# Kernel optimization log

Measured on AMD Instinct MI355X. Metric: run time of the kernel, lower is better.

The kernel has to match this reference:

```python
import jax, jax.numpy as jnp
import numpy as np

NEG_INF = -1e30  # stands in for float('-inf'); avoids nan in masked softmax edge cases


def setup_inputs() -> dict:
    key = jax.random.key(0)
    ks = jax.random.split(key, 6)
    B, N, MD, QD, AD = 64, 512, 1024, 1024, 1024
    stdv_m = 1.0 / np.sqrt(MD)
    stdv_q = 1.0 / np.sqrt(QD)
    stdv_a = 1.0 / np.sqrt(AD)
    return {
        "memory_values": jax.random.normal(ks[0], (B, N, MD), dtype=jnp.float32),
        "mask": jax.random.randint(ks[1], (B, N), 0, 2, dtype=jnp.int32),
        "query": jax.random.normal(ks[2], (B, QD), dtype=jnp.float32),
        "Wh": jax.random.uniform(ks[3], (MD, AD), jnp.float32, -stdv_m, stdv_m),
        "Ws": jax.random.uniform(ks[4], (QD, AD), jnp.float32, -stdv_q, stdv_q),
        "v": jax.random.uniform(ks[5], (AD, 1), jnp.float32, -stdv_a, stdv_a),
    }


def reference(memory_values, mask, query, Wh, Ws, v):
    # Et(i) = tanh(Hi*Wh + St*Ws) @ v ; At = softmax(Et) with masking
    tq = query @ Ws                                   # (B, AD)
    h = jnp.tanh(memory_values @ Wh + tq[:, None, :])  # (B, N, AD)
    logits = jnp.squeeze(h @ v, axis=-1)              # (B, N)

    maskf = mask.astype(logits.dtype)
    # no_cells[b] == 1 iff every cell in row b is masked out
    no_cells = jnp.prod(1.0 - maskf, axis=1, keepdims=True)  # (B, 1)
    suppress = jnp.where(maskf == 0, NEG_INF, 0.0)
    suppress = jnp.where(no_cells == 1.0, 0.0, suppress)
    weights = jax.nn.softmax(logits + suppress, axis=-1)
    weights = jnp.where(no_cells == 1.0, 0.0, weights)

    context = jnp.einsum("bn,bnd->bd", weights, memory_values)
    return context
```

## Files before the change

### kernel.cpp

```cpp
#include <hip/hip_runtime.h>
#include <cstdint>
#include <cstddef>

typedef float floatx4 __attribute__((ext_vector_type(4)));
typedef _Float16 half8_t __attribute__((ext_vector_type(8)));
typedef _Float16 half2_t __attribute__((ext_vector_type(2)));

#define AS1 __attribute__((address_space(1)))
#define AS3 __attribute__((address_space(3)))

__device__ __forceinline__ void glds16(const void* g, void* l) {
  __builtin_amdgcn_global_load_lds((const AS1 void*)g, (AS3 void*)l, 16, 0, 0);
}

__device__ __forceinline__ half2_t pkrtz(float a, float b) {
  return __builtin_bit_cast(half2_t, __builtin_amdgcn_cvt_pkrtz(a, b));
}

__device__ __forceinline__ float fast_tanh(float x) {
  float e2 = __expf(2.f * x);
  return 1.f - 2.f * __builtin_amdgcn_rcpf(e2 + 1.f);
}

__global__ void kp_cvt(const float* __restrict__ mem, _Float16* __restrict__ memh) {
  size_t i = ((size_t)(blockIdx.x << 8) + threadIdx.x) << 3;
  floatx4 a = *(const floatx4*)(mem + i);
  floatx4 b = *(const floatx4*)(mem + i + 4);
  union { half2_t h2[4]; half8_t h8; } u;
  u.h2[0] = half2_t{(_Float16)a[0], (_Float16)a[1]};
  u.h2[1] = half2_t{(_Float16)a[2], (_Float16)a[3]};
  u.h2[2] = half2_t{(_Float16)b[0], (_Float16)b[1]};
  u.h2[3] = half2_t{(_Float16)b[2], (_Float16)b[3]};
  *(half8_t*)(memh + i) = u.h8;
}

__global__ void k0_transpose(const float* __restrict__ Wh, _Float16* __restrict__ WhT) {
  __shared__ float t[64][65];
  int k0 = blockIdx.y << 6, n0 = blockIdx.x << 6;
  int tx = threadIdx.x, ty = threadIdx.y;
  #pragma unroll
  for (int r = ty; r < 64; r += 4) t[r][tx] = Wh[(size_t)(k0 + r) * 1024 + n0 + tx];
  __syncthreads();
  #pragma unroll
  for (int r = ty; r < 64; r += 4)
    WhT[(size_t)(n0 + r) * 1024 + k0 + tx] = (_Float16)t[tx][r];
}

__global__ __launch_bounds__(256) void k1a_tq(const float* __restrict__ q,
                                              const float* __restrict__ Ws,
                                              float* __restrict__ tqp) {
  __shared__ float qts[64][68];
  __shared__ float wss[64][68];
  const int db = blockIdx.x << 6, kb = blockIdx.y << 6;
  const int tid = threadIdx.x;
  for (int idx = tid; idx < 4096; idx += 256) {
    int b = idx >> 6, kk = idx & 63;
    qts[kk][b] = q[(b << 10) + kb + kk];
  }
  for (int idx = tid; idx < 4096; idx += 256) {
    int kk = idx >> 6, dd = idx & 63;
    wss[kk][dd] = Ws[(size_t)(kb + kk) * 1024 + db + dd];
  }
  __syncthreads();
  const int bq = tid >> 4, dq = tid & 15;
  floatx4 acc[4] = {{0.f, 0.f, 0.f, 0.f}, {0.f, 0.f, 0.f, 0.f},
                    {0.f, 0.f, 0.f, 0.f}, {0.f, 0.f, 0.f, 0.f}};
  for (int kk = 0; kk < 64; ++kk) {
    floatx4 wv = *(const floatx4*)&wss[kk][dq << 2];
    floatx4 qv = *(const floatx4*)&qts[kk][bq << 2];
    #pragma unroll
    for (int bb = 0; bb < 4; ++bb) acc[bb] += qv[bb] * wv;
  }
  #pragma unroll
  for (int bb = 0; bb < 4; ++bb) {
    int b = (bq << 2) + bb;
    *(floatx4*)(tqp + ((size_t)blockIdx.y << 16) + (b << 10) + db + (dq << 2)) = acc[bb];
  }
}

__global__ void k1b_red(const float* __restrict__ tqp, float* __restrict__ tq) {
  int i = (blockIdx.x << 8) + threadIdx.x;
  float s = 0.f;
  #pragma unroll
  for (int kc = 0; kc < 16; ++kc) s += tqp[((size_t)kc << 16) + i];
  tq[i] = s;
}

__global__ __launch_bounds__(256) void k1_tq(const float* __restrict__ q,
                                             const float* __restrict__ Ws,
                                             float* __restrict__ tq) {
  __shared__ float qs[1024];
  __shared__ float red[4][64];
  int b = blockIdx.y;
  int d0 = blockIdx.x << 6;
  int dl = threadIdx.x & 63, kg = threadIdx.x >> 6;
  for (int k = threadIdx.x; k < 1024; k += 256) qs[k] = q[(b << 10) + k];
  __syncthreads();
  float acc = 0.f;
  int kbase = kg << 8;
  #pragma unroll 8
  for (int k = 0; k < 256; ++k)
    acc += qs[kbase + k] * Ws[(size_t)(kbase + k) * 1024 + d0 + dl];
  red[kg][dl] = acc;
  __syncthreads();
  if (kg == 0)
    tq[(b << 10) + d0 + dl] = red[0][dl] + red[1][dl] + red[2][dl] + red[3][dl];
}

__global__ __launch_bounds__(256, 2) void k2_gemm_h(
    const _Float16* __restrict__ Ah, const _Float16* __restrict__ BT,
    const float* __restrict__ tq, const float* __restrict__ v,
    float* __restrict__ partials) {
  __shared__ _Float16 As[128 * 32];
  __shared__ _Float16 Bs[128 * 32];
  const int bid = blockIdx.x;
  const int mtile = ((bid >> 6) << 3) | (bid & 7);
  const int nblk = (bid >> 3) & 7;
  const int m0 = mtile << 7, n0 = nblk << 7;
  const int tid = threadIdx.x;
  const int w = tid >> 6, lane = tid & 63;
  const int wm = w >> 1, wn = w & 1, quad = lane >> 4, l15 = lane & 15;

  floatx4 acc[4][4];
  #pragma unroll
  for (int i = 0; i < 4; ++i)
    #pragma unroll
    for (int j = 0; j < 4; ++j) acc[i][j] = floatx4{0.f, 0.f, 0.f, 0.f};

  const _Float16 *gA[2], *gB[2];
  _Float16 *lA[2], *lB[2];
  #pragma unroll
  for (int t = 0; t < 2; ++t) {
    int L = (t << 8) + (w << 6) + lane;
    int row = L >> 2, jj = L & 3;
    int j = (jj - row - (row >> 2)) & 3;
    gA[t] = Ah + (size_t)(m0 + row) * 1024 + (j << 3);
    gB[t] = BT + (size_t)(n0 + row) * 1024 + (j << 3);
    lA[t] = As + (t << 11) + (w << 9);
    lB[t] = Bs + (t << 11) + (w << 9);
  }

  const half8_t *aaddr[4], *baddr[4];
  #pragma unroll
  for (int i = 0; i < 4; ++i) {
    int ar = (wm << 6) + (i << 4) + l15;
    aaddr[i] = (const half8_t*)(As + (ar << 5) + (((quad + ar + (ar >> 2)) & 3) << 3));
    int br = (wn << 6) + (i << 4) + l15;
    baddr[i] = (const half8_t*)(Bs + (br << 5) + (((quad + br + (br >> 2)) & 3) << 3));
  }

  for (int k0 = 0; k0 < 1024; k0 += 32) {
    __syncthreads();
    glds16(gA[0] + k0, lA[0]);
    glds16(gA[1] + k0, lA[1]);
    glds16(gB[0] + k0, lB[0]);
    glds16(gB[1] + k0, lB[1]);
    __syncthreads();
    half8_t af[4], bfr[4];
    #pragma unroll
    for (int i = 0; i < 4; ++i) af[i] = *aaddr[i];
    #pragma unroll
    for (int j = 0; j < 4; ++j) bfr[j] = *baddr[j];
    #pragma unroll
    for (int i = 0; i < 4; ++i)
      #pragma unroll
      for (int j = 0; j < 4; ++j)
        acc[i][j] = __builtin_amdgcn_mfma_f32_16x16x32_f16(af[i], bfr[j], acc[i][j], 0, 0, 0);
  }

  const int b = m0 >> 9;
  const int colbase = n0 + (wn << 6) + l15;
  float tqv[4], vv[4];
  #pragma unroll
  for (int j = 0; j < 4; ++j) {
    int n = colbase + (j << 4);
    tqv[j] = tq[(b << 10) + n];
    vv[j] = v[n];
  }
  #pragma unroll
  for (int i = 0; i < 4; ++i) {
    #pragma unroll
    for (int r = 0; r < 4; ++r) {
      float s = 0.f;
      #pragma unroll
      for (int j = 0; j < 4; ++j) s += fast_tanh(acc[i][j][r] + tqv[j]) * vv[j];
      s += __shfl_xor(s, 1);
      s += __shfl_xor(s, 2);
      s += __shfl_xor(s, 4);
      s += __shfl_xor(s, 8);
      if (l15 == 0) {
        int m = m0 + (wm << 6) + (i << 4) + (quad << 2) + r;
        partials[m * 16 + (nblk << 1) + wn] = s;
      }
    }
  }
}

__global__ __launch_bounds__(256, 2) void k2_gemm_f32(
    const float* __restrict__ A, const _Float16* __restrict__ BT,
    const float* __restrict__ tq, const float* __restrict__ v,
    float* __restrict__ partials) {
  __shared__ float As[128 * 32];
  __shared__ _Float16 Bs[128 * 32];
  const int bid = blockIdx.x;
  const int mtile = ((bid >> 6) << 3) | (bid & 7);
  const int nblk = (bid >> 3) & 7;
  const int m0 = mtile << 7, n0 = nblk << 7;
  const int tid = threadIdx.x;
  const int w = tid >> 6, lane = tid & 63;
  const int wm = w >> 1, wn = w & 1, quad = lane >> 4, l15 = lane & 15;

  floatx4 acc[4][4];
  #pragma unroll
  for (int i = 0; i < 4; ++i)
    #pragma unroll
    for (int j = 0; j < 4; ++j) acc[i][j] = floatx4{0.f, 0.f, 0.f, 0.f};

  const float* gA[4];
  float* lA[4];
  #pragma unroll
  for (int t = 0; t < 4; ++t) {
    int L = (t << 8) + (w << 6) + lane;
    int row = L >> 3, jj = L & 7;
    int j = (jj - row) & 7;
    gA[t] = A + (size_t)(m0 + row) * 1024 + (j << 2);
    lA[t] = As + (t << 10) + (w << 8);
  }
  const _Float16* gB[2];
  _Float16* lB[2];
  #pragma unroll
  for (int t = 0; t < 2; ++t) {
    int L = (t << 8) + (w << 6) + lane;
    int row = L >> 2, jj = L & 3;
    int j = (jj - row - (row >> 2)) & 3;
    gB[t] = BT + (size_t)(n0 + row) * 1024 + (j << 3);
    lB[t] = Bs + (t << 11) + (w << 9);
  }
  const floatx4* aaddr[4][2];
  #pragma unroll
  for (int i = 0; i < 4; ++i) {
    int row = (wm << 6) + (i << 4) + l15;
    #pragma unroll
    for (int h = 0; h < 2; ++h) {
      int pos = ((quad << 1) + h + row) & 7;
      aaddr[i][h] = (const floatx4*)(As + (row << 5) + (pos << 2));
    }
  }
  const half8_t* baddr[4];
  #pragma unroll
  for (int j = 0; j < 4; ++j) {
    int row = (wn << 6) + (j << 4) + l15;
    int pos = (quad + row + (row >> 2)) & 3;
    baddr[j] = (const half8_t*)(Bs + (row << 5) + (pos << 3));
  }
  for (int k0 = 0; k0 < 1024; k0 += 32) {
    __syncthreads();
    glds16(gA[0] + k0, lA[0]);
    glds16(gA[1] + k0, lA[1]);
    glds16(gA[2] + k0, lA[2]);
    glds16(gA[3] + k0, lA[3]);
    glds16(gB[0] + k0, lB[0]);
    glds16(gB[1] + k0, lB[1]);
    __syncthreads();
    half8_t af[4], bfr[4];
    #pragma unroll
    for (int i = 0; i < 4; ++i) {
      floatx4 x = *aaddr[i][0], y = *aaddr[i][1];
      union { half2_t h2[4]; half8_t h8; } u;
      u.h2[0] = pkrtz(x[0], x[1]);
      u.h2[1] = pkrtz(x[2], x[3]);
      u.h2[2] = pkrtz(y[0], y[1]);
      u.h2[3] = pkrtz(y[2], y[3]);
      af[i] = u.h8;
    }
    #pragma unroll
    for (int j = 0; j < 4; ++j) bfr[j] = *baddr[j];
    #pragma unroll
    for (int i = 0; i < 4; ++i)
      #pragma unroll
      for (int j = 0; j < 4; ++j)
        acc[i][j] = __builtin_amdgcn_mfma_f32_16x16x32_f16(af[i], bfr[j], acc[i][j], 0, 0, 0);
  }
  const int b = m0 >> 9;
  const int colbase = n0 + (wn << 6) + l15;
  float tqv[4], vv[4];
  #pragma unroll
  for (int j = 0; j < 4; ++j) {
    int n = colbase + (j << 4);
    tqv[j] = tq[(b << 10) + n];
    vv[j] = v[n];
  }
  #pragma unroll
  for (int i = 0; i < 4; ++i) {
    #pragma unroll
    for (int r = 0; r < 4; ++r) {
      float s = 0.f;
      #pragma unroll
      for (int j = 0; j < 4; ++j) s += fast_tanh(acc[i][j][r] + tqv[j]) * vv[j];
      s += __shfl_xor(s, 1);
      s += __shfl_xor(s, 2);
      s += __shfl_xor(s, 4);
      s += __shfl_xor(s, 8);
      if (l15 == 0) {
        int m = m0 + (wm << 6) + (i << 4) + (quad << 2) + r;
        partials[m * 16 + (nblk << 1) + wn] = s;
      }
    }
  }
}

__global__ __launch_bounds__(512) void k3_softmax(const float* __restrict__ partials,
                                                  const int* __restrict__ mask,
                                                  float* __restrict__ weights) {
  int b = blockIdx.x;
  int n = threadIdx.x;
  int m = (b << 9) + n;
  float s = 0.f;
  #pragma unroll
  for (int i = 0; i < 16; ++i) s += partials[m * 16 + i];
  int mk = mask[m];
  float logit = mk ? s : -1e30f;
  __shared__ float red[8];
  float x = logit;
  #pragma unroll
  for (int off = 32; off > 0; off >>= 1) x = fmaxf(x, __shfl_xor(x, off));
  if ((n & 63) == 0) red[n >> 6] = x;
  __syncthreads();
  float mx = red[0];
  #pragma unroll
  for (int i = 1; i < 8; ++i) mx = fmaxf(mx, red[i]);
  float e = mk ? __expf(logit - mx) : 0.f;
  float ss = e;
  #pragma unroll
  for (int off = 32; off > 0; off >>= 1) ss += __shfl_xor(ss, off);
  __syncthreads();
  if ((n & 63) == 0) red[n >> 6] = ss;
  __syncthreads();
  float tot = 0.f;
  #pragma unroll
  for (int i = 0; i < 8; ++i) tot += red[i];
  weights[m] = (tot > 0.f) ? e / tot : 0.f;
}

__global__ void k4_ctx_h(const _Float16* __restrict__ memh,
                         const float* __restrict__ weights, float* __restrict__ ctxp) {
  int nc = blockIdx.x, b = blockIdx.y;
  int d = threadIdx.x << 3;
  float acc[8] = {0.f, 0.f, 0.f, 0.f, 0.f, 0.f, 0.f, 0.f};
  int nbase = nc << 5;
  for (int n = nbase; n < nbase + 32; ++n) {
    float wv = weights[(b << 9) + n];
    half8_t x = *(const half8_t*)(memh + ((size_t)((b << 9) + n) << 10) + d);
    #pragma unroll
    for (int k = 0; k < 8; ++k) acc[k] += wv * (float)x[k];
  }
  float* o = ctxp + ((size_t)((b << 4) + nc) << 10) + d;
  #pragma unroll
  for (int k = 0; k < 8; ++k) o[k] = acc[k];
}

__global__ void k5_reduce16(const float* __restrict__ ctxp, float* __restrict__ out) {
  int i = (blockIdx.x << 8) + threadIdx.x;
  int b = i >> 10, d = i & 1023;
  float s = 0.f;
  #pragma unroll
  for (int cc = 0; cc < 16; ++cc) s += ctxp[((size_t)((b << 4) + cc) << 10) + d];
  out[i] = s;
}

__global__ void k4_ctx_f32(const float* __restrict__ mem, const float* __restrict__ weights,
                           float* __restrict__ ctxp) {
  int nc = blockIdx.x, b = blockIdx.y;
  int d = threadIdx.x << 3;
  floatx4 a0 = {0.f, 0.f, 0.f, 0.f}, a1 = {0.f, 0.f, 0.f, 0.f};
  int nbase = nc << 6;
  for (int n = nbase; n < nbase + 64; ++n) {
    float wv = weights[(b << 9) + n];
    const floatx4* p = (const floatx4*)(mem + ((size_t)((b << 9) + n) << 10) + d);
    a0 += wv * p[0];
    a1 += wv * p[1];
  }
  floatx4* o = (floatx4*)(ctxp + ((size_t)((b << 3) + nc) << 10) + d);
  o[0] = a0;
  o[1] = a1;
}

__global__ void k5_reduce8(const float* __restrict__ ctxp, float* __restrict__ out) {
  int i = (blockIdx.x << 8) + threadIdx.x;
  int b = i >> 10, d = i & 1023;
  float s = 0.f;
  #pragma unroll
  for (int cc = 0; cc < 8; ++cc) s += ctxp[((size_t)((b << 3) + cc) << 10) + d];
  out[i] = s;
}

extern "C" void kernel_launch(void* const* d_in, const int* in_sizes, int n_in,
                              void* d_out, int out_size, void* d_ws, size_t ws_size,
                              hipStream_t stream) {
  const float* mem = (const float*)d_in[0];
  const int* mask = (const int*)d_in[1];
  const float* query = (const float*)d_in[2];
  const float* Wh = (const float*)d_in[3];
  const float* Ws = (const float*)d_in[4];
  const float* v = (const float*)d_in[5];
  float* out = (float*)d_out;

  char* ws = (char*)d_ws;
  const size_t need16 = (73ull << 20);

  if (ws_size >= need16) {
    _Float16* memh = (_Float16*)ws;
    _Float16* WhT = (_Float16*)(ws + (64ull << 20));
    float* partials = (float*)(ws + (66ull << 20));
    float* tq = (float*)(ws + (68ull << 20));
    float* weights = (float*)(ws + (68ull << 20) + (256 << 10));
    float* ctxp = (float*)(ws + (69ull << 20));
    float* tqp = ctxp;

    kp_cvt<<<16384, 256, 0, stream>>>(mem, memh);
    k0_transpose<<<dim3(16, 16), dim3(64, 4), 0, stream>>>(Wh, WhT);
    k1a_tq<<<dim3(16, 16), 256, 0, stream>>>(query, Ws, tqp);
    k1b_red<<<256, 256, 0, stream>>>(tqp, tq);
    k2_gemm_h<<<2048, 256, 0, stream>>>(memh, WhT, tq, v, partials);
    k3_softmax<<<64, 512, 0, stream>>>(partials, mask, weights);
    k4_ctx_h<<<dim3(16, 64), 128, 0, stream>>>(memh, weights, ctxp);
    k5_reduce16<<<256, 256, 0, stream>>>(ctxp, out);
  } else {
    _Float16* WhT = (_Float16*)ws;
    float* partials = (float*)(ws + ((size_t)2 << 20));
    float* tq = (float*)(ws + ((size_t)4 << 20));
    float* weights = (float*)(ws + ((size_t)4 << 20) + (256 << 10));
    float* ctxp = (float*)(ws + ((size_t)9 << 19));

    k0_transpose<<<dim3(16, 16), dim3(64, 4), 0, stream>>>(Wh, WhT);
    k1_tq<<<dim3(16, 64), 256, 0, stream>>>(query, Ws, tq);
    k2_gemm_f32<<<2048, 256, 0, stream>>>(mem, WhT, tq, v, partials);
    k3_softmax<<<64, 512, 0, stream>>>(partials, mask, weights);
    k4_ctx_f32<<<dim3(8, 64), 128, 0, stream>>>(mem, weights, ctxp);
    k5_reduce8<<<256, 256, 0, stream>>>(ctxp, out);
  }
}
```

Measured before the change: 338.5 us.

## Fuse prep kernels into one launch and fold tq reduction into GEMM

Merges the fp16 conversion of memory, the Wh transpose and the partial query projection into a single heterogeneous kernel that dispatches on block index, removing three launches and the separate tq reduction kernel. The GEMM kernel now sums the 16 tq partials itself in its prologue, which adds some redundant global reads per block. The context kernel is reshaped to 256 threads with 64 rows per chunk and 8 partials, which halves the final reduction input. The transpose blocks are now serialized over 16 k-tiles each, so only 16 blocks do that work and they may form a long tail.

```diff
diff --git a/kernel.cpp b/kernel.cpp
--- a/kernel.cpp
+++ b/kernel.cpp
@@ -4,6 +4,7 @@
 
 typedef float floatx4 __attribute__((ext_vector_type(4)));
 typedef _Float16 half8_t __attribute__((ext_vector_type(8)));
+typedef _Float16 half4_t __attribute__((ext_vector_type(4)));
 typedef _Float16 half2_t __attribute__((ext_vector_type(2)));
 
 #define AS1 __attribute__((address_space(1)))
@@ -22,94 +23,77 @@
   return 1.f - 2.f * __builtin_amdgcn_rcpf(e2 + 1.f);
 }
 
-__global__ void kp_cvt(const float* __restrict__ mem, _Float16* __restrict__ memh) {
-  size_t i = ((size_t)(blockIdx.x << 8) + threadIdx.x) << 3;
-  floatx4 a = *(const floatx4*)(mem + i);
-  floatx4 b = *(const floatx4*)(mem + i + 4);
-  union { half2_t h2[4]; half8_t h8; } u;
-  u.h2[0] = half2_t{(_Float16)a[0], (_Float16)a[1]};
-  u.h2[1] = half2_t{(_Float16)a[2], (_Float16)a[3]};
-  u.h2[2] = half2_t{(_Float16)b[0], (_Float16)b[1]};
-  u.h2[3] = half2_t{(_Float16)b[2], (_Float16)b[3]};
-  *(half8_t*)(memh + i) = u.h8;
-}
-
-__global__ void k0_transpose(const float* __restrict__ Wh, _Float16* __restrict__ WhT) {
-  __shared__ float t[64][65];
-  int k0 = blockIdx.y << 6, n0 = blockIdx.x << 6;
-  int tx = threadIdx.x, ty = threadIdx.y;
-  #pragma unroll
-  for (int r = ty; r < 64; r += 4) t[r][tx] = Wh[(size_t)(k0 + r) * 1024 + n0 + tx];
-  __syncthreads();
-  #pragma unroll
-  for (int r = ty; r < 64; r += 4)
-    WhT[(size_t)(n0 + r) * 1024 + k0 + tx] = (_Float16)t[tx][r];
-}
-
-__global__ __launch_bounds__(256) void k1a_tq(const float* __restrict__ q,
-                                              const float* __restrict__ Ws,
-                                              float* __restrict__ tqp) {
-  __shared__ float qts[64][68];
-  __shared__ float wss[64][68];
-  const int db = blockIdx.x << 6, kb = blockIdx.y << 6;
+__global__ __launch_bounds__(256) void k_prep(
+    const float* __restrict__ mem, const float* __restrict__ Wh,
+    const float* __restrict__ q, const float* __restrict__ Ws,
+    _Float16* __restrict__ memh, _Float16* __restrict__ WhT,
+    float* __restrict__ tqp) {
+  __shared__ union {
+    float t[64][65];
+    struct { float qts[64][68]; float wss[64][68]; } k1;
+  } sm;
+  const int bx = blockIdx.x;
   const int tid = threadIdx.x;
-  for (int idx = tid; idx < 4096; idx += 256) {
-    int b = idx >> 6, kk = idx & 63;
-    qts[kk][b] = q[(b << 10) + kb + kk];
-  }
-  for (int idx = tid; idx < 4096; idx += 256) {
-    int kk = idx >> 6, dd = idx & 63;
-    wss[kk][dd] = Ws[(size_t)(kb + kk) * 1024 + db + dd];
-  }
-  __syncthreads();
-  const int bq = tid >> 4, dq = tid & 15;
-  floatx4 acc[4] = {{0.f, 0.f, 0.f, 0.f}, {0.f, 0.f, 0.f, 0.f},
-                    {0.f, 0.f, 0.f, 0.f}, {0.f, 0.f, 0.f, 0.f}};
-  for (int kk = 0; kk < 64; ++kk) {
-    floatx4 wv = *(const floatx4*)&wss[kk][dq << 2];
-    floatx4 qv = *(const floatx4*)&qts[kk][bq << 2];
-    #pragma unroll
-    for (int bb = 0; bb < 4; ++bb) acc[bb] += qv[bb] * wv;
-  }
-  #pragma unroll
-  for (int bb = 0; bb < 4; ++bb) {
-    int b = (bq << 2) + bb;
-    *(floatx4*)(tqp + ((size_t)blockIdx.y << 16) + (b << 10) + db + (dq << 2)) = acc[bb];
-  }
-}
-
-__global__ void k1b_red(const float* __restrict__ tqp, float* __restrict__ tq) {
-  int i = (blockIdx.x << 8) + threadIdx.x;
-  float s = 0.f;
-  #pragma unroll
-  for (int kc = 0; kc < 16; ++kc) s += tqp[((size_t)kc << 16) + i];
-  tq[i] = s;
-}
-
-__global__ __launch_bounds__(256) void k1_tq(const float* __restrict__ q,
-                                             const float* __restrict__ Ws,
-                                             float* __restrict__ tq) {
-  __shared__ float qs[1024];
-  __shared__ float red[4][64];
-  int b = blockIdx.y;
-  int d0 = blockIdx.x << 6;
-  int dl = threadIdx.x & 63, kg = threadIdx.x >> 6;
-  for (int k = threadIdx.x; k < 1024; k += 256) qs[k] = q[(b << 10) + k];
-  __syncthreads();
-  float acc = 0.f;
-  int kbase = kg << 8;
-  #pragma unroll 8
-  for (int k = 0; k < 256; ++k)
-    acc += qs[kbase + k] * Ws[(size_t)(kbase + k) * 1024 + d0 + dl];
-  red[kg][dl] = acc;
-  __syncthreads();
-  if (kg == 0)
-    tq[(b << 10) + d0 + dl] = red[0][dl] + red[1][dl] + red[2][dl] + red[3][dl];
+
+  if (bx < 8192) {
+    size_t base = ((size_t)bx << 12);
+    #pragma unroll
+    for (int p = 0; p < 4; ++p) {
+      size_t i = base + (p << 10) + (tid << 2);
+      floatx4 x = *(const floatx4*)(mem + i);
+      half4_t h = {(_Float16)x[0], (_Float16)x[1], (_Float16)x[2], (_Float16)x[3]};
+      *(half4_t*)(memh + i) = h;
+    }
+  } else if (bx < 8208) {
+    const int n0 = (bx - 8192) << 6;
+    const int c = tid & 63, rr = tid >> 6;
+    for (int kt = 0; kt < 16; ++kt) {
+      int k0 = kt << 6;
+      #pragma unroll
+      for (int i = 0; i < 16; ++i) {
+        int r = (i << 2) + rr;
+        sm.t[r][c] = Wh[(size_t)(k0 + r) * 1024 + n0 + c];
+      }
+      __syncthreads();
+      #pragma unroll
+      for (int i = 0; i < 16; ++i) {
+        int r = (i << 2) + rr;
+        WhT[(size_t)(n0 + r) * 1024 + k0 + c] = (_Float16)sm.t[c][r];
+      }
+      __syncthreads();
+    }
+  } else {
+    const int bid2 = bx - 8208;
+    const int db = (bid2 & 15) << 6, kb = (bid2 >> 4) << 6;
+    for (int idx = tid; idx < 4096; idx += 256) {
+      int b = idx >> 6, kk = idx & 63;
+      sm.k1.qts[kk][b] = q[(b << 10) + kb + kk];
+    }
+    for (int idx = tid; idx < 4096; idx += 256) {
+      int kk = idx >> 6, dd = idx & 63;
+      sm.k1.wss[kk][dd] = Ws[(size_t)(kb + kk) * 1024 + db + dd];
+    }
+    __syncthreads();
+    const int bq = tid >> 4, dq = tid & 15;
+    floatx4 acc[4] = {{0.f, 0.f, 0.f, 0.f}, {0.f, 0.f, 0.f, 0.f},
+                      {0.f, 0.f, 0.f, 0.f}, {0.f, 0.f, 0.f, 0.f}};
+    for (int kk = 0; kk < 64; ++kk) {
+      floatx4 wv = *(const floatx4*)&sm.k1.wss[kk][dq << 2];
+      floatx4 qv = *(const floatx4*)&sm.k1.qts[kk][bq << 2];
+      #pragma unroll
+      for (int bb = 0; bb < 4; ++bb) acc[bb] += qv[bb] * wv;
+    }
+    #pragma unroll
+    for (int bb = 0; bb < 4; ++bb) {
+      int b = (bq << 2) + bb;
+      *(floatx4*)(tqp + ((size_t)(bid2 >> 4) << 16) + (b << 10) + db + (dq << 2)) = acc[bb];
+    }
+  }
 }
 
 __global__ __launch_bounds__(256, 2) void k2_gemm_h(
     const _Float16* __restrict__ Ah, const _Float16* __restrict__ BT,
-    const float* __restrict__ tq, const float* __restrict__ v,
+    const float* __restrict__ tqp, const float* __restrict__ v,
     float* __restrict__ partials) {
   __shared__ _Float16 As[128 * 32];
   __shared__ _Float16 Bs[128 * 32];
@@ -121,6 +105,19 @@
   const int w = tid >> 6, lane = tid & 63;
   const int wm = w >> 1, wn = w & 1, quad = lane >> 4, l15 = lane & 15;
 
+  const int b = m0 >> 9;
+  const int colbase = n0 + (wn << 6) + l15;
+  float tqv[4], vv[4];
+  #pragma unroll
+  for (int j = 0; j < 4; ++j) {
+    int n = colbase + (j << 4);
+    float s = 0.f;
+    #pragma unroll
+    for (int p = 0; p < 16; ++p) s += tqp[(p << 16) + (b << 10) + n];
+    tqv[j] = s;
+    vv[j] = v[n];
+  }
+
   floatx4 acc[4][4];
   #pragma unroll
   for (int i = 0; i < 4; ++i)
@@ -168,15 +165,6 @@
         acc[i][j] = __builtin_amdgcn_mfma_f32_16x16x32_f16(af[i], bfr[j], acc[i][j], 0, 0, 0);
   }
 
-  const int b = m0 >> 9;
-  const int colbase = n0 + (wn << 6) + l15;
-  float tqv[4], vv[4];
-  #pragma unroll
-  for (int j = 0; j < 4; ++j) {
-    int n = colbase + (j << 4);
-    tqv[j] = tq[(b << 10) + n];
-    vv[j] = v[n];
-  }
   #pragma unroll
   for (int i = 0; i < 4; ++i) {
     #pragma unroll
@@ -194,6 +182,99 @@
       }
     }
   }
+}
+
+__global__ __launch_bounds__(512) void k3_softmax(const float* __restrict__ partials,
+                                                  const int* __restrict__ mask,
+                                                  float* __restrict__ weights) {
+  int b = blockIdx.x;
+  int n = threadIdx.x;
+  int m = (b << 9) + n;
+  float s = 0.f;
+  #pragma unroll
+  for (int i = 0; i < 16; ++i) s += partials[m * 16 + i];
+  int mk = mask[m];
+  float logit = mk ? s : -1e30f;
+  __shared__ float red[8];
+  float x = logit;
+  #pragma unroll
+  for (int off = 32; off > 0; off >>= 1) x = fmaxf(x, __shfl_xor(x, off));
+  if ((n & 63) == 0) red[n >> 6] = x;
+  __syncthreads();
+  float mx = red[0];
+  #pragma unroll
+  for (int i = 1; i < 8; ++i) mx = fmaxf(mx, red[i]);
+  float e = mk ? __expf(logit - mx) : 0.f;
+  float ss = e;
+  #pragma unroll
+  for (int off = 32; off > 0; off >>= 1) ss += __shfl_xor(ss, off);
+  __syncthreads();
+  if ((n & 63) == 0) red[n >> 6] = ss;
+  __syncthreads();
+  float tot = 0.f;
+  #pragma unroll
+  for (int i = 0; i < 8; ++i) tot += red[i];
+  weights[m] = (tot > 0.f) ? e / tot : 0.f;
+}
+
+__global__ __launch_bounds__(256) void k4_ctx_h(const _Float16* __restrict__ memh,
+                                                const float* __restrict__ weights,
+                                                float* __restrict__ ctxp) {
+  int nc = blockIdx.x, b = blockIdx.y;
+  int d = threadIdx.x << 2;
+  float a0 = 0.f, a1 = 0.f, a2 = 0.f, a3 = 0.f;
+  int nbase = nc << 6;
+  for (int n = nbase; n < nbase + 64; ++n) {
+    float wv = weights[(b << 9) + n];
+    half4_t x = *(const half4_t*)(memh + ((size_t)((b << 9) + n) << 10) + d);
+    a0 += wv * (float)x[0];
+    a1 += wv * (float)x[1];
+    a2 += wv * (float)x[2];
+    a3 += wv * (float)x[3];
+  }
+  *(floatx4*)(ctxp + ((size_t)((b << 3) + nc) << 10) + d) = floatx4{a0, a1, a2, a3};
+}
+
+__global__ void k5_reduce8(const float* __restrict__ ctxp, float* __restrict__ out) {
+  int i = (blockIdx.x << 8) + threadIdx.x;
+  int b = i >> 10, d = i & 1023;
+  float s = 0.f;
+  #pragma unroll
+  for (int cc = 0; cc < 8; ++cc) s += ctxp[((size_t)((b << 3) + cc) << 10) + d];
+  out[i] = s;
+}
+
+__global__ void k0_transpose(const float* __restrict__ Wh, _Float16* __restrict__ WhT) {
+  __shared__ float t[64][65];
+  int k0 = blockIdx.y << 6, n0 = blockIdx.x << 6;
+  int tx = threadIdx.x, ty = threadIdx.y;
+  #pragma unroll
+  for (int r = ty; r < 64; r += 4) t[r][tx] = Wh[(size_t)(k0 + r) * 1024 + n0 + tx];
+  __syncthreads();
+  #pragma unroll
+  for (int r = ty; r < 64; r += 4)
+    WhT[(size_t)(n0 + r) * 1024 + k0 + tx] = (_Float16)t[tx][r];
+}
+
+__global__ __launch_bounds__(256) void k1_tq(const float* __restrict__ q,
+                                             const float* __restrict__ Ws,
+                                             float* __restrict__ tq) {
+  __shared__ float qs[1024];
+  __shared__ float red[4][64];
+  int b = blockIdx.y;
+  int d0 = blockIdx.x << 6;
+  int dl = threadIdx.x & 63, kg = threadIdx.x >> 6;
+  for (int k = threadIdx.x; k < 1024; k += 256) qs[k] = q[(b << 10) + k];
+  __syncthreads();
+  float acc = 0.f;
+  int kbase = kg << 8;
+  #pragma unroll 8
+  for (int k = 0; k < 256; ++k)
+    acc += qs[kbase + k] * Ws[(size_t)(kbase + k) * 1024 + d0 + dl];
+  red[kg][dl] = acc;
+  __syncthreads();
+  if (kg == 0)
+    tq[(b << 10) + d0 + dl] = red[0][dl] + red[1][dl] + red[2][dl] + red[3][dl];
 }
 
 __global__ __launch_bounds__(256, 2) void k2_gemm_f32(
@@ -209,13 +290,11 @@
   const int tid = threadIdx.x;
   const int w = tid >> 6, lane = tid & 63;
   const int wm = w >> 1, wn = w & 1, quad = lane >> 4, l15 = lane & 15;
-
   floatx4 acc[4][4];
   #pragma unroll
   for (int i = 0; i < 4; ++i)
     #pragma unroll
     for (int j = 0; j < 4; ++j) acc[i][j] = floatx4{0.f, 0.f, 0.f, 0.f};
-
   const float* gA[4];
   float* lA[4];
   #pragma unroll
@@ -307,65 +386,6 @@
       }
     }
   }
-}
-
-__global__ __launch_bounds__(512) void k3_softmax(const float* __restrict__ partials,
-                                                  const int* __restrict__ mask,
-                                                  float* __restrict__ weights) {
-  int b = blockIdx.x;
-  int n = threadIdx.x;
-  int m = (b << 9) + n;
-  float s = 0.f;
-  #pragma unroll
-  for (int i = 0; i < 16; ++i) s += partials[m * 16 + i];
-  int mk = mask[m];
-  float logit = mk ? s : -1e30f;
-  __shared__ float red[8];
-  float x = logit;
-  #pragma unroll
-  for (int off = 32; off > 0; off >>= 1) x = fmaxf(x, __shfl_xor(x, off));
-  if ((n & 63) == 0) red[n >> 6] = x;
-  __syncthreads();
-  float mx = red[0];
-  #pragma unroll
-  for (int i = 1; i < 8; ++i) mx = fmaxf(mx, red[i]);
-  float e = mk ? __expf(logit - mx) : 0.f;
-  float ss = e;
-  #pragma unroll
-  for (int off = 32; off > 0; off >>= 1) ss += __shfl_xor(ss, off);
-  __syncthreads();
-  if ((n & 63) == 0) red[n >> 6] = ss;
-  __syncthreads();
-  float tot = 0.f;
-  #pragma unroll
-  for (int i = 0; i < 8; ++i) tot += red[i];
-  weights[m] = (tot > 0.f) ? e / tot : 0.f;
-}
-
-__global__ void k4_ctx_h(const _Float16* __restrict__ memh,
-                         const float* __restrict__ weights, float* __restrict__ ctxp) {
-  int nc = blockIdx.x, b = blockIdx.y;
-  int d = threadIdx.x << 3;
-  float acc[8] = {0.f, 0.f, 0.f, 0.f, 0.f, 0.f, 0.f, 0.f};
-  int nbase = nc << 5;
-  for (int n = nbase; n < nbase + 32; ++n) {
-    float wv = weights[(b << 9) + n];
-    half8_t x = *(const half8_t*)(memh + ((size_t)((b << 9) + n) << 10) + d);
-    #pragma unroll
-    for (int k = 0; k < 8; ++k) acc[k] += wv * (float)x[k];
-  }
-  float* o = ctxp + ((size_t)((b << 4) + nc) << 10) + d;
-  #pragma unroll
-  for (int k = 0; k < 8; ++k) o[k] = acc[k];
-}
-
-__global__ void k5_reduce16(const float* __restrict__ ctxp, float* __restrict__ out) {
-  int i = (blockIdx.x << 8) + threadIdx.x;
-  int b = i >> 10, d = i & 1023;
-  float s = 0.f;
-  #pragma unroll
-  for (int cc = 0; cc < 16; ++cc) s += ctxp[((size_t)((b << 4) + cc) << 10) + d];
-  out[i] = s;
 }
 
 __global__ void k4_ctx_f32(const float* __restrict__ mem, const float* __restrict__ weights,
@@ -385,15 +405,6 @@
   o[1] = a1;
 }
 
-__global__ void k5_reduce8(const float* __restrict__ ctxp, float* __restrict__ out) {
-  int i = (blockIdx.x << 8) + threadIdx.x;
-  int b = i >> 10, d = i & 1023;
-  float s = 0.f;
-  #pragma unroll
-  for (int cc = 0; cc < 8; ++cc) s += ctxp[((size_t)((b << 3) + cc) << 10) + d];
-  out[i] = s;
-}
-
 extern "C" void kernel_launch(void* const* d_in, const int* in_sizes, int n_in,
                               void* d_out, int out_size, void* d_ws, size_t ws_size,
                               hipStream_t stream) {
@@ -412,19 +423,15 @@
     _Float16* memh = (_Float16*)ws;
     _Float16* WhT = (_Float16*)(ws + (64ull << 20));
     float* partials = (float*)(ws + (66ull << 20));
-    float* tq = (float*)(ws + (68ull << 20));
-    float* weights = (float*)(ws + (68ull << 20) + (256 << 10));
-    float* ctxp = (float*)(ws + (69ull << 20));
-    float* tqp = ctxp;
-
-    kp_cvt<<<16384, 256, 0, stream>>>(mem, memh);
-    k0_transpose<<<dim3(16, 16), dim3(64, 4), 0, stream>>>(Wh, WhT);
-    k1a_tq<<<dim3(16, 16), 256, 0, stream>>>(query, Ws, tqp);
-    k1b_red<<<256, 256, 0, stream>>>(tqp, tq);
-    k2_gemm_h<<<2048, 256, 0, stream>>>(memh, WhT, tq, v, partials);
+    float* tqp = (float*)(ws + (68ull << 20));
+    float* ctxp = tqp;
+    float* weights = (float*)(ws + (72ull << 20));
+
+    k_prep<<<8464, 256, 0, stream>>>(mem, Wh, query, Ws, memh, WhT, tqp);
+    k2_gemm_h<<<2048, 256, 0, stream>>>(memh, WhT, tqp, v, partials);
     k3_softmax<<<64, 512, 0, stream>>>(partials, mask, weights);
-    k4_ctx_h<<<dim3(16, 64), 128, 0, stream>>>(memh, weights, ctxp);
-    k5_reduce16<<<256, 256, 0, stream>>>(ctxp, out);
+    k4_ctx_h<<<dim3(8, 64), 256, 0, stream>>>(memh, weights, ctxp);
+    k5_reduce8<<<256, 256, 0, stream>>>(ctxp, out);
   } else {
     _Float16* WhT = (_Float16*)ws;
     float* partials = (float*)(ws + ((size_t)2 << 20));
```

Result: no change. 338.4 us (-0.0%).
